# Optimization experiments

Measured on AMD Instinct MI355X. Metric: run time of the kernel, lower is better.

Reference implementation:

```python
import jax, jax.numpy as jnp
import numpy as np

N = 50000       # nodes per subgraph scale
E = 800000      # edges per subgraph scale
B = 4096        # number of subgraphs (graphs in the batch)
IN, HID, OUT = 64, 64, 32
NE = 8          # num_experts
EMB = 64        # emb_dim per expert
E2 = 131072     # graph-level edges for distortion loss


def setup_inputs() -> dict:
    key = jax.random.key(0)
    ks = jax.random.split(key, 16)
    inv = lambda d: 1.0 / np.sqrt(d)
    return {
        "subgraph_x0": jax.random.normal(ks[0], (N, IN), jnp.float32),
        "subgraph_x1": jax.random.normal(ks[1], (N, IN), jnp.float32),
        "W1": jax.random.normal(ks[2], (IN, HID), jnp.float32) * inv(IN),
        "b1": jnp.zeros((HID,), jnp.float32),
        "W2": jax.random.normal(ks[3], (HID, OUT), jnp.float32) * inv(HID),
        "b2": jnp.zeros((OUT,), jnp.float32),
        "Wc": jax.random.normal(ks[4], (OUT * 2, NE), jnp.float32) * inv(OUT * 2),
        "bc": jnp.zeros((NE,), jnp.float32),
        "embeddings": jax.random.normal(ks[5], (B, NE * EMB), jnp.float32),
        # precomputed shortest-path distances per graph edge (positive)
        "dis": jax.random.uniform(ks[6], (E2,), jnp.float32) * 1.5 + 0.5,
        "edge_index0": jax.random.randint(ks[7], (2, E), 0, N, jnp.int32),
        "edge_index1": jax.random.randint(ks[8], (2, E), 0, N, jnp.int32),
        "batch0": jnp.sort(jax.random.randint(ks[9], (N,), 0, B, jnp.int32)),
        "batch1": jnp.sort(jax.random.randint(ks[10], (N,), 0, B, jnp.int32)),
        "edge_index2": jax.random.randint(ks[11], (2, E2), 0, B, jnp.int32),
        "emb_dim": EMB,
    }


def _gcn_conv(x, W, b, src, dst, n):
    """PyG GCNConv: D^{-1/2}(A+I)D^{-1/2} X W + b, with self-loops."""
    xw = x @ W  # [n, out]
    ones = jnp.ones(src.shape, xw.dtype)
    deg = jax.ops.segment_sum(ones, dst, num_segments=n) + 1.0  # self-loop degree
    dinv = jax.lax.rsqrt(deg)  # [n]
    norm = dinv[src] * dinv[dst]  # [E]
    agg = jax.ops.segment_sum(xw[src] * norm[:, None], dst, num_segments=n)
    agg = agg + (dinv * dinv)[:, None] * xw  # self-loop messages
    return agg + b


def _mean_pool(x, batch, num_graphs):
    s = jax.ops.segment_sum(x, batch, num_segments=num_graphs)
    cnt = jax.ops.segment_sum(jnp.ones((x.shape[0],), x.dtype), batch,
                              num_segments=num_graphs)
    return s / jnp.maximum(cnt, 1.0)[:, None]


def _encode_scale(x, edge_index, batch, W1, b1, W2, b2, num_graphs):
    src, dst = edge_index[0], edge_index[1]
    n = x.shape[0]
    h = _gcn_conv(x, W1, b1, src, dst, n)
    h = _gcn_conv(h, W2, b2, src, dst, n)
    return _mean_pool(h, batch, num_graphs)


def reference(subgraph_x0, subgraph_x1, W1, b1, W2, b2, Wc, bc,
              embeddings, dis, edge_index0, edge_index1,
              batch0, batch1, edge_index2, emb_dim):
    num_graphs = embeddings.shape[0]
    x0 = _encode_scale(subgraph_x0, edge_index0, batch0, W1, b1, W2, b2, num_graphs)
    x1 = _encode_scale(subgraph_x1, edge_index1, batch1, W1, b1, W2, b2, num_graphs)
    x = jnp.concatenate([x0, x1], axis=-1)  # [B, 2*OUT]
    gate = jax.nn.softmax(x @ Wc + bc, axis=-1)  # temperature = 1.0

    # distortion loss over graph-level edges
    s, d = edge_index2[0], edge_index2[1]
    e = edge_index2.shape[1]
    diff = (embeddings[s] - embeddings[d]) ** 2  # [E2, NE*emb_dim]
    diff = diff.reshape(e, diff.shape[1] // emb_dim, emb_dim).sum(axis=2)  # [E2, NE]
    weights = jax.nn.softmax(gate[s] * gate[d], axis=1)  # [E2, NE]
    dsum = jnp.sum(diff * weights, axis=-1)  # [E2]
    loss_distortion = jnp.mean(jnp.abs(dsum / dis - 1.0))
    return gate, loss_distortion
```

## Files before the change

### kernel.cpp

```cpp
#include <hip/hip_runtime.h>
#include <math.h>

constexpr int IN_F  = 64;
constexpr int HID_F = 64;
constexpr int OUT_F = 32;
constexpr int NEXP  = 8;
constexpr int EMB   = 64;


__global__ void zero_f32_kernel(float* __restrict__ p, long long n) {
    long long i = (long long)blockIdx.x * blockDim.x + threadIdx.x;
    long long stride = (long long)gridDim.x * blockDim.x;
    for (; i < n; i += stride) p[i] = 0.0f;
}

__global__ void zero_i32_kernel(int* __restrict__ p, long long n) {
    long long i = (long long)blockIdx.x * blockDim.x + threadIdx.x;
    long long stride = (long long)gridDim.x * blockDim.x;
    for (; i < n; i += stride) p[i] = 0;
}

__global__ __launch_bounds__(1024)
void w12_kernel(const float* __restrict__ W1, const float* __restrict__ W2,
                const float* __restrict__ b1,
                float* __restrict__ W12, float* __restrict__ c1)
{
    __shared__ float sW2[HID_F * OUT_F];
    const int tid = threadIdx.x;
    for (int i = tid; i < HID_F * OUT_F; i += 1024) sW2[i] = W2[i];
    __syncthreads();
    for (int idx = tid; idx < IN_F * OUT_F; idx += 1024) {
        int i = idx >> 5, j = idx & 31;
        float acc = 0.0f;
#pragma unroll
        for (int k = 0; k < HID_F; ++k) acc += W1[i * HID_F + k] * sW2[k * OUT_F + j];
        W12[idx] = acc;
    }
    if (tid < OUT_F) {
        float acc = 0.0f;
#pragma unroll
        for (int k = 0; k < HID_F; ++k) acc += b1[k] * sW2[k * OUT_F + tid];
        c1[tid] = acc;
    }
}

__global__ void hist2_kernel(const int* __restrict__ ei0, const int* __restrict__ ei1,
                             int* __restrict__ counts, int E, int N)
{
    int e = blockIdx.x * blockDim.x + threadIdx.x;
    if (e >= 2 * E) return;
    int d = (e < E) ? ei0[E + e] : (ei1[E + (e - E)] + N);
    atomicAdd(&counts[d], 1);
}

__global__ __launch_bounds__(1024)
void scan1_kernel(const int* __restrict__ counts, int* __restrict__ lexcl,
                  int* __restrict__ partials, int N)
{
    __shared__ int wsum[16];
    const int tid  = threadIdx.x;
    const int lane = tid & 63;
    const int wv   = tid >> 6;
    const int i    = blockIdx.x * 1024 + tid;

    int v = (i < N) ? counts[i] : 0;
    int x = v;
#pragma unroll
    for (int off = 1; off < 64; off <<= 1) {
        int t = __shfl_up(x, off);
        if (lane >= off) x += t;
    }
    if (lane == 63) wsum[wv] = x;
    __syncthreads();
    int woff = 0;
    for (int w = 0; w < wv; ++w) woff += wsum[w];
    if (i < N) lexcl[i] = woff + x - v;
    if (tid == 1023) partials[blockIdx.x] = woff + x;
}

__global__ __launch_bounds__(1024)
void scan2_kernel(int* __restrict__ partials, int NB)
{
    __shared__ int wsum[16];
    const int tid  = threadIdx.x;
    const int lane = tid & 63;
    const int wv   = tid >> 6;
    int v = (tid < NB) ? partials[tid] : 0;
    int x = v;
#pragma unroll
    for (int off = 1; off < 64; off <<= 1) {
        int t = __shfl_up(x, off);
        if (lane >= off) x += t;
    }
    if (lane == 63) wsum[wv] = x;
    __syncthreads();
    int woff = 0;
    for (int w = 0; w < wv; ++w) woff += wsum[w];
    if (tid < NB) partials[tid] = woff + x - v;
}

__global__ void scan3_kernel(const int* __restrict__ lexcl, const int* __restrict__ partials,
                             const int* __restrict__ counts,
                             int* __restrict__ offsets, int* __restrict__ cursor,
                             float* __restrict__ dinv, int n2, int e2tot)
{
    int i = blockIdx.x * blockDim.x + threadIdx.x;
    if (i >= n2) return;
    int o = lexcl[i] + partials[i >> 10];
    offsets[i] = o;
    cursor[i]  = o;
    dinv[i] = rsqrtf((float)counts[i] + 1.0f);
    if (i == 0) offsets[n2] = e2tot;
}

__global__ __launch_bounds__(256)
void scatter2_shard_kernel(const int* __restrict__ ei0, const int* __restrict__ ei1,
                           int* __restrict__ cursor, int* __restrict__ csr_src,
                           int E, int N, int n2)
{
    const int shard   = blockIdx.x & 7;
    const int bid     = blockIdx.x >> 3;
    const int nblocks = gridDim.x >> 3;
    const int lo = (int)(((long long)n2 * shard) >> 3);
    const int hi = (int)(((long long)n2 * (shard + 1)) >> 3);

    long long start  = (long long)bid * blockDim.x + threadIdx.x;
    long long stride = (long long)nblocks * blockDim.x;
    const long long e2 = 2LL * E;
    for (long long e = start; e < e2; e += stride) {
        int s, d;
        if (e < E) { s = ei0[e];                 d = ei0[E + e]; }
        else       { s = ei1[e - E] + N;         d = ei1[E + (e - E)] + N; }
        if (d >= lo && d < hi) {
            int pos = atomicAdd(&cursor[d], 1);
            csr_src[pos] = s;
        }
    }
}

__global__ __launch_bounds__(256)
void gemm_ys2_kernel(const float* __restrict__ x0, const float* __restrict__ x1,
                     const float* __restrict__ W12, const float* __restrict__ dinv,
                     float* __restrict__ Ys, int N, int n2)
{
    __shared__ float Ws[IN_F * OUT_F];
    __shared__ float xs[8 * IN_F];
    const int tid = threadIdx.x;

    for (int i = tid; i < IN_F * OUT_F; i += 256) Ws[i] = W12[i];
    const int row0 = blockIdx.x * 8;
    for (int i = tid; i < 8 * IN_F; i += 256) {
        int r = i >> 6;
        int rr = row0 + r;
        float v = 0.0f;
        if (rr < n2) {
            v = (rr < N) ? x0[(size_t)rr * IN_F + (i & 63)]
                         : x1[(size_t)(rr - N) * IN_F + (i & 63)];
        }
        xs[i] = v;
    }
    __syncthreads();

    const int r = tid >> 5;
    const int c = tid & 31;
    const int row = row0 + r;
    if (row >= n2) return;

    float acc = 0.0f;
#pragma unroll
    for (int k = 0; k < IN_F; ++k) acc += xs[r * IN_F + k] * Ws[k * OUT_F + c];

    Ys[(size_t)row * OUT_F + c] = acc * dinv[row];
}

template<int MODE>
__global__ __launch_bounds__(256)
void csr_agg32_kernel(const int* __restrict__ csr_src, const int* __restrict__ offsets,
                      const float* __restrict__ in, const float* __restrict__ dinv,
                      float* __restrict__ sdsum, const float* __restrict__ c1,
                      const float* __restrict__ b2,
                      float* __restrict__ out, int n)
{
    constexpr int F = OUT_F;
    const int lane = threadIdx.x & 63;
    const int wid  = (blockIdx.x * (blockDim.x >> 6)) + (threadIdx.x >> 6);
    const int sub  = lane >> 5;
    const int f    = lane & 31;
    const int node = wid * 2 + sub;
    const int lbase = sub * F;

    const bool valid = (node < n);
    const int nc   = valid ? node : 0;
    const int off0 = offsets[nc];
    const int off1 = valid ? offsets[nc + 1] : off0;

    float acc0 = valid ? in[(size_t)nc * F + f] : 0.0f;
    float acc1 = 0.0f, acc2 = 0.0f, acc3 = 0.0f;
    float dsum = 0.0f;
    for (int k = off0; k < off1; k += F) {
        int nk = off1 - k; if (nk > F) nk = F;
        int sj = (f < nk) ? csr_src[k + f] : 0;
        if (MODE == 0) {
            float dv = dinv[sj];
            dsum += (f < nk) ? dv : 0.0f;
        }
        int t = 0;
        for (; t + 8 <= nk; t += 8) {
            int s0 = __shfl(sj, lbase + t);
            int s1 = __shfl(sj, lbase + t + 1);
            int s2 = __shfl(sj, lbase + t + 2);
            int s3 = __shfl(sj, lbase + t + 3);
            int s4 = __shfl(sj, lbase + t + 4);
            int s5 = __shfl(sj, lbase + t + 5);
            int s6 = __shfl(sj, lbase + t + 6);
            int s7 = __shfl(sj, lbase + t + 7);
            float v0 = in[(size_t)s0 * F + f];
            float v1 = in[(size_t)s1 * F + f];
            float v2 = in[(size_t)s2 * F + f];
            float v3 = in[(size_t)s3 * F + f];
            float v4 = in[(size_t)s4 * F + f];
            float v5 = in[(size_t)s5 * F + f];
            float v6 = in[(size_t)s6 * F + f];
            float v7 = in[(size_t)s7 * F + f];
            acc0 += v0 + v4;
            acc1 += v1 + v5;
            acc2 += v2 + v6;
            acc3 += v3 + v7;
        }
        for (; t < nk; ++t) {
            int s = __shfl(sj, lbase + t);
            acc0 += in[(size_t)s * F + f];
        }
    }
    if (MODE == 0) {
#pragma unroll
        for (int off = 1; off < 32; off <<= 1) dsum += __shfl_xor(dsum, off);
    }
    if (valid) {
        float di = dinv[node];
        float s = (acc0 + acc1) + (acc2 + acc3);
        if (MODE == 0) {
            out[(size_t)node * F + f] = di * di * s;
            if (f == 0) sdsum[node] = dsum;
        } else {
            float t = di * (di + sdsum[node]);
            out[(size_t)node * F + f] = di * s + t * c1[f] + b2[f];
        }
    }
}

__global__ void pool_sum2_kernel(const float* __restrict__ h,
                                 const int* __restrict__ bat0, const int* __restrict__ bat1,
                                 float* __restrict__ pooled, float* __restrict__ cnt,
                                 int N, int n2, int B)
{
    int t = blockIdx.x * blockDim.x + threadIdx.x;
    int i = t >> 5;
    int f = t & 31;
    if (i >= n2) return;
    int g = (i < N) ? bat0[i] : (bat1[i - N] + B);
    atomicAdd(&pooled[(size_t)g * OUT_F + f], h[(size_t)i * OUT_F + f]);
    if (f == 0) atomicAdd(&cnt[g], 1.0f);
}

__global__ void pool_div_kernel(float* __restrict__ pooled, const float* __restrict__ cnt, int B2)
{
    int t = blockIdx.x * blockDim.x + threadIdx.x;
    if (t >= B2 * OUT_F) return;
    int g = t >> 5;
    pooled[t] /= fmaxf(cnt[g], 1.0f);
}

__global__ void gate_kernel(const float* __restrict__ p0, const float* __restrict__ p1,
                            const float* __restrict__ Wc, const float* __restrict__ bc,
                            float* __restrict__ gate, int B)
{
    int g = blockIdx.x * blockDim.x + threadIdx.x;
    if (g >= B) return;
    float xv[2 * OUT_F];
#pragma unroll
    for (int k = 0; k < OUT_F; ++k) xv[k] = p0[(size_t)g * OUT_F + k];
#pragma unroll
    for (int k = 0; k < OUT_F; ++k) xv[OUT_F + k] = p1[(size_t)g * OUT_F + k];

    float lg[NEXP];
    float m = -1e30f;
#pragma unroll
    for (int e = 0; e < NEXP; ++e) {
        float acc = bc[e];
#pragma unroll
        for (int k = 0; k < 2 * OUT_F; ++k) acc += xv[k] * Wc[k * NEXP + e];
        lg[e] = acc;
        m = fmaxf(m, acc);
    }
    float se = 0.0f;
#pragma unroll
    for (int e = 0; e < NEXP; ++e) { lg[e] = expf(lg[e] - m); se += lg[e]; }
    float inv = 1.0f / se;
#pragma unroll
    for (int e = 0; e < NEXP; ++e) gate[(size_t)g * NEXP + e] = lg[e] * inv;
}

__global__ void zero_scalar_kernel(float* p) { *p = 0.0f; }

__global__ void histD_kernel(const int* __restrict__ s_idx, int* __restrict__ cntD, int E2) {
    int e = blockIdx.x * blockDim.x + threadIdx.x;
    if (e >= E2) return;
    atomicAdd(&cntD[s_idx[e]], 1);
}

__global__ void combineD_kernel(const int* __restrict__ lexclD, const int* __restrict__ partialsD,
                                int* __restrict__ offD, int* __restrict__ curD, int B, int E2)
{
    int i = blockIdx.x * blockDim.x + threadIdx.x;
    if (i >= B) return;
    int o = lexclD[i] + partialsD[i >> 10];
    offD[i] = o;
    curD[i] = o;
    if (i == 0) offD[B] = E2;
}

__global__ void scatterD_kernel(const int* __restrict__ s_idx, const int* __restrict__ d_idx,
                                const float* __restrict__ dis,
                                int* __restrict__ curD, int* __restrict__ dD,
                                float* __restrict__ disD, int E2)
{
    int e = blockIdx.x * blockDim.x + threadIdx.x;
    if (e >= E2) return;
    int s = s_idx[e];
    int pos = atomicAdd(&curD[s], 1);
    dD[pos] = d_idx[e];
    disD[pos] = dis[e];
}

__global__ __launch_bounds__(256)
void distortion3_kernel(const float* __restrict__ emb, const float* __restrict__ gate,
                        const int* __restrict__ offD, const int* __restrict__ dD,
                        const float* __restrict__ disD,
                        float* __restrict__ loss, int B, int E2)
{
    const int s    = (blockIdx.x * (blockDim.x >> 6)) + (threadIdx.x >> 6);
    const int lane = threadIdx.x & 63;
    const int half = lane >> 5;
    const int hl   = lane & 31;
    const int g    = hl >> 4;
    if (s >= B) return;

    const float4* emb4  = (const float4*)emb;
    const float4* gate4 = (const float4*)gate;

    const float4* es = emb4 + (size_t)s * 128;
    float4 a0 = es[hl];
    float4 a1 = es[hl + 32];
    float4 a2 = es[hl + 64];
    float4 a3 = es[hl + 96];
    float4 gs0 = gate4[(size_t)s * 2];
    float4 gs1 = gate4[(size_t)s * 2 + 1];

    float lsum = 0.0f;
    const int j0 = offD[s];
    const int j1 = offD[s + 1];
    for (int j = j0 + half; j < j1; j += 2) {
        int d = dD[j];
        float dv = disD[j];
        const float4* ed = emb4 + (size_t)d * 128;
        float4 b0 = ed[hl];
        float4 b1 = ed[hl + 32];
        float4 b2 = ed[hl + 64];
        float4 b3 = ed[hl + 96];
        float4 gd0 = gate4[(size_t)d * 2];
        float4 gd1 = gate4[(size_t)d * 2 + 1];

        float dx;
        float pa, pb, pc, pd;
        dx = a0.x - b0.x; pa  = dx * dx;
        dx = a0.y - b0.y; pa += dx * dx;
        dx = a0.z - b0.z; pa += dx * dx;
        dx = a0.w - b0.w; pa += dx * dx;
        dx = a1.x - b1.x; pb  = dx * dx;
        dx = a1.y - b1.y; pb += dx * dx;
        dx = a1.z - b1.z; pb += dx * dx;
        dx = a1.w - b1.w; pb += dx * dx;
        dx = a2.x - b2.x; pc  = dx * dx;
        dx = a2.y - b2.y; pc += dx * dx;
        dx = a2.z - b2.z; pc += dx * dx;
        dx = a2.w - b2.w; pc += dx * dx;
        dx = a3.x - b3.x; pd  = dx * dx;
        dx = a3.y - b3.y; pd += dx * dx;
        dx = a3.z - b3.z; pd += dx * dx;
        dx = a3.w - b3.w; pd += dx * dx;

#pragma unroll
        for (int off = 1; off < 16; off <<= 1) {
            pa += __shfl_xor(pa, off);
            pb += __shfl_xor(pb, off);
            pc += __shfl_xor(pc, off);
            pd += __shfl_xor(pd, off);
        }

        float gp[NEXP] = { gs0.x * gd0.x, gs0.y * gd0.y, gs0.z * gd0.z, gs0.w * gd0.w,
                           gs1.x * gd1.x, gs1.y * gd1.y, gs1.z * gd1.z, gs1.w * gd1.w };
        float m = gp[0];
#pragma unroll
        for (int j2 = 1; j2 < NEXP; ++j2) m = fmaxf(m, gp[j2]);
        float se = 0.0f;
#pragma unroll
        for (int j2 = 0; j2 < NEXP; ++j2) { gp[j2] = expf(gp[j2] - m); se += gp[j2]; }

        float v = pa * gp[g] + pb * gp[g + 2] + pc * gp[g + 4] + pd * gp[g + 6];
        v += __shfl_xor(v, 16);

        lsum += fabsf((v / se) / dv - 1.0f);
    }
    float other = __shfl_xor(lsum, 32);
    if (lane == 0) atomicAdd(loss, (lsum + other) / (float)E2);
}

extern "C" void kernel_launch(void* const* d_in, const int* in_sizes, int n_in,
                              void* d_out, int out_size, void* d_ws, size_t ws_size,
                              hipStream_t stream)
{
    const float* x0   = (const float*)d_in[0];
    const float* x1   = (const float*)d_in[1];
    const float* W1   = (const float*)d_in[2];
    const float* b1   = (const float*)d_in[3];
    const float* W2   = (const float*)d_in[4];
    const float* b2   = (const float*)d_in[5];
    const float* Wc   = (const float*)d_in[6];
    const float* bc   = (const float*)d_in[7];
    const float* emb  = (const float*)d_in[8];
    const float* dis  = (const float*)d_in[9];
    const int*   ei0  = (const int*)d_in[10];
    const int*   ei1  = (const int*)d_in[11];
    const int*   bat0 = (const int*)d_in[12];
    const int*   bat1 = (const int*)d_in[13];
    const int*   ei2  = (const int*)d_in[14];

    const int N  = in_sizes[0] / IN_F;
    const int E  = in_sizes[10] / 2;
    const int B  = in_sizes[8] / (NEXP * EMB);
    const int E2 = in_sizes[14] / 2;
    const int n2 = 2 * N;

    float* gate_out = (float*)d_out;
    float* loss_out = gate_out + (size_t)B * NEXP;

    float* ws      = (float*)d_ws;
    float* dinv    = ws;
    float* Ys      = dinv + n2;
    float* Zs      = Ys + (size_t)n2 * OUT_F;
    float* sdsum   = Zs + (size_t)n2 * OUT_F;
    float* pooled  = sdsum + n2;
    float* cnt     = pooled + (size_t)2 * B * OUT_F;
    float* W12     = cnt + 2 * B;
    float* c1      = W12 + IN_F * OUT_F;
    float* disD    = c1 + OUT_F;
    int*   iws     = (int*)(disD + E2);
    int*   counts  = iws;
    int*   offsets = counts + n2;
    int*   cursor  = offsets + n2 + 1;
    int*   csr_src = cursor + n2;
    int*   lexcl   = csr_src + 2 * E;
    int*   partials= lexcl + n2;
    int*   cntD    = partials + 1024;
    int*   lexclD  = cntD + B;
    int*   partialsD = lexclD + B;
    int*   offD    = partialsD + 16;
    int*   curD    = offD + B + 1;
    int*   dD      = curD + B;

    const int TB = 256;
    const int zgrid = 512;
    const int NB2 = (n2 + 1023) / 1024;
    const int NBD = (B + 1023) / 1024;

    w12_kernel<<<1, 1024, 0, stream>>>(W1, W2, b1, W12, c1);

    zero_i32_kernel<<<zgrid, TB, 0, stream>>>(counts, n2);
    hist2_kernel<<<(2 * E + TB - 1) / TB, TB, 0, stream>>>(ei0, ei1, counts, E, N);
    scan1_kernel<<<NB2, 1024, 0, stream>>>(counts, lexcl, partials, n2);
    scan2_kernel<<<1, 1024, 0, stream>>>(partials, NB2);
    scan3_kernel<<<(n2 + TB - 1) / TB, TB, 0, stream>>>(lexcl, partials, counts,
                                                        offsets, cursor, dinv, n2, 2 * E);
    scatter2_shard_kernel<<<1024, TB, 0, stream>>>(ei0, ei1, cursor, csr_src, E, N, n2);

    zero_i32_kernel<<<zgrid, TB, 0, stream>>>(cntD, B);
    histD_kernel<<<(E2 + TB - 1) / TB, TB, 0, stream>>>(ei2, cntD, E2);
    scan1_kernel<<<NBD, 1024, 0, stream>>>(cntD, lexclD, partialsD, B);
    scan2_kernel<<<1, 1024, 0, stream>>>(partialsD, NBD);
    combineD_kernel<<<(B + TB - 1) / TB, TB, 0, stream>>>(lexclD, partialsD, offD, curD, B, E2);
    scatterD_kernel<<<(E2 + TB - 1) / TB, TB, 0, stream>>>(ei2, ei2 + E2, dis,
                                                           curD, dD, disD, E2);

    gemm_ys2_kernel<<<(n2 + 7) / 8, 256, 0, stream>>>(x0, x1, W12, dinv, Ys, N, n2);
    csr_agg32_kernel<0><<<(n2 + 7) / 8, TB, 0, stream>>>(csr_src, offsets, Ys, dinv,
                                                         sdsum, nullptr, nullptr, Zs, n2);
    csr_agg32_kernel<1><<<(n2 + 7) / 8, TB, 0, stream>>>(csr_src, offsets, Zs, dinv,
                                                         sdsum, c1, b2, Ys, n2);

    zero_f32_kernel<<<zgrid, TB, 0, stream>>>(pooled, (long long)2 * B * OUT_F);
    zero_f32_kernel<<<zgrid, TB, 0, stream>>>(cnt, 2 * B);
    pool_sum2_kernel<<<((n2 * 32) + TB - 1) / TB, TB, 0, stream>>>(Ys, bat0, bat1,
                                                                   pooled, cnt, N, n2, B);
    pool_div_kernel<<<((2 * B * OUT_F) + TB - 1) / TB, TB, 0, stream>>>(pooled, cnt, 2 * B);

    gate_kernel<<<(B + TB - 1) / TB, TB, 0, stream>>>(pooled, pooled + (size_t)B * OUT_F,
                                                      Wc, bc, gate_out, B);

    zero_scalar_kernel<<<1, 1, 0, stream>>>(loss_out);
    distortion3_kernel<<<(B + 3) / 4, TB, 0, stream>>>(emb, gate_out, offD, dD, disD,
                                                       loss_out, B, E2);
}
```

Measured before the change: 419.8 us.

## Bucket distortion edges by destination quarter and pin quarters to XCDs

Graph-level edges are now bucketed by (destination quarter, source) instead of source alone, using a 4*B-entry histogram, scan and scatter. The distortion kernel launches a fixed 1024 blocks and derives a quarter and half-range from blockIdx&7. Blocks on the same XCD (assuming round-robin block placement) then gather destination embeddings from one quarter of the table, which should improve per-XCD L2 hit rates. In exchange, each source's embedding row and gate are reloaded up to four times, and the bucketing scan is four times larger.

```diff
diff --git a/kernel.cpp b/kernel.cpp
--- a/kernel.cpp
+++ b/kernel.cpp
@@ -303,114 +303,131 @@
 
 __global__ void zero_scalar_kernel(float* p) { *p = 0.0f; }
 
-__global__ void histD_kernel(const int* __restrict__ s_idx, int* __restrict__ cntD, int E2) {
+__global__ void histK_kernel(const int* __restrict__ s_idx, const int* __restrict__ d_idx,
+                             int* __restrict__ histK, int E2, int B, int quarter)
+{
     int e = blockIdx.x * blockDim.x + threadIdx.x;
     if (e >= E2) return;
-    atomicAdd(&cntD[s_idx[e]], 1);
-}
-
-__global__ void combineD_kernel(const int* __restrict__ lexclD, const int* __restrict__ partialsD,
-                                int* __restrict__ offD, int* __restrict__ curD, int B, int E2)
+    int qd = d_idx[e] / quarter; if (qd > 3) qd = 3;
+    atomicAdd(&histK[qd * B + s_idx[e]], 1);
+}
+
+__global__ void combineK_kernel(const int* __restrict__ lexclK, const int* __restrict__ partialsK,
+                                int* __restrict__ offK, int* __restrict__ curK, int nk, int E2)
 {
     int i = blockIdx.x * blockDim.x + threadIdx.x;
-    if (i >= B) return;
-    int o = lexclD[i] + partialsD[i >> 10];
-    offD[i] = o;
-    curD[i] = o;
-    if (i == 0) offD[B] = E2;
-}
-
-__global__ void scatterD_kernel(const int* __restrict__ s_idx, const int* __restrict__ d_idx,
+    if (i >= nk) return;
+    int o = lexclK[i] + partialsK[i >> 10];
+    offK[i] = o;
+    curK[i] = o;
+    if (i == 0) offK[nk] = E2;
+}
+
+__global__ void scatterK_kernel(const int* __restrict__ s_idx, const int* __restrict__ d_idx,
                                 const float* __restrict__ dis,
-                                int* __restrict__ curD, int* __restrict__ dD,
-                                float* __restrict__ disD, int E2)
+                                int* __restrict__ curK, int* __restrict__ dD,
+                                float* __restrict__ disD, int E2, int B, int quarter)
 {
     int e = blockIdx.x * blockDim.x + threadIdx.x;
     if (e >= E2) return;
-    int s = s_idx[e];
-    int pos = atomicAdd(&curD[s], 1);
-    dD[pos] = d_idx[e];
+    int d = d_idx[e];
+    int qd = d / quarter; if (qd > 3) qd = 3;
+    int pos = atomicAdd(&curK[qd * B + s_idx[e]], 1);
+    dD[pos] = d;
     disD[pos] = dis[e];
 }
 
 __global__ __launch_bounds__(256)
-void distortion3_kernel(const float* __restrict__ emb, const float* __restrict__ gate,
-                        const int* __restrict__ offD, const int* __restrict__ dD,
+void distortion5_kernel(const float* __restrict__ emb, const float* __restrict__ gate,
+                        const int* __restrict__ offK, const int* __restrict__ dD,
                         const float* __restrict__ disD,
                         float* __restrict__ loss, int B, int E2)
 {
-    const int s    = (blockIdx.x * (blockDim.x >> 6)) + (threadIdx.x >> 6);
     const int lane = threadIdx.x & 63;
     const int half = lane >> 5;
     const int hl   = lane & 31;
     const int g    = hl >> 4;
-    if (s >= B) return;
+    const int xcd  = blockIdx.x & 7;
+    const int bid  = blockIdx.x >> 3;
+    const int wv   = threadIdx.x >> 6;
+    const int wIdx = bid * 4 + wv;
+
+    const int qd   = xcd >> 1;
+    const int sh   = xcd & 1;
+    const int halfB = B >> 1;
+    const int k0 = qd * B + sh * halfB;
+    const int k1 = qd * B + (sh ? B : halfB);
 
     const float4* emb4  = (const float4*)emb;
     const float4* gate4 = (const float4*)gate;
 
-    const float4* es = emb4 + (size_t)s * 128;
-    float4 a0 = es[hl];
-    float4 a1 = es[hl + 32];
-    float4 a2 = es[hl + 64];
-    float4 a3 = es[hl + 96];
-    float4 gs0 = gate4[(size_t)s * 2];
-    float4 gs1 = gate4[(size_t)s * 2 + 1];
-
     float lsum = 0.0f;
-    const int j0 = offD[s];
-    const int j1 = offD[s + 1];
-    for (int j = j0 + half; j < j1; j += 2) {
-        int d = dD[j];
-        float dv = disD[j];
-        const float4* ed = emb4 + (size_t)d * 128;
-        float4 b0 = ed[hl];
-        float4 b1 = ed[hl + 32];
-        float4 b2 = ed[hl + 64];
-        float4 b3 = ed[hl + 96];
-        float4 gd0 = gate4[(size_t)d * 2];
-        float4 gd1 = gate4[(size_t)d * 2 + 1];
-
-        float dx;
-        float pa, pb, pc, pd;
-        dx = a0.x - b0.x; pa  = dx * dx;
-        dx = a0.y - b0.y; pa += dx * dx;
-        dx = a0.z - b0.z; pa += dx * dx;
-        dx = a0.w - b0.w; pa += dx * dx;
-        dx = a1.x - b1.x; pb  = dx * dx;
-        dx = a1.y - b1.y; pb += dx * dx;
-        dx = a1.z - b1.z; pb += dx * dx;
-        dx = a1.w - b1.w; pb += dx * dx;
-        dx = a2.x - b2.x; pc  = dx * dx;
-        dx = a2.y - b2.y; pc += dx * dx;
-        dx = a2.z - b2.z; pc += dx * dx;
-        dx = a2.w - b2.w; pc += dx * dx;
-        dx = a3.x - b3.x; pd  = dx * dx;
-        dx = a3.y - b3.y; pd += dx * dx;
-        dx = a3.z - b3.z; pd += dx * dx;
-        dx = a3.w - b3.w; pd += dx * dx;
-
-#pragma unroll
-        for (int off = 1; off < 16; off <<= 1) {
-            pa += __shfl_xor(pa, off);
-            pb += __shfl_xor(pb, off);
-            pc += __shfl_xor(pc, off);
-            pd += __shfl_xor(pd, off);
-        }
-
-        float gp[NEXP] = { gs0.x * gd0.x, gs0.y * gd0.y, gs0.z * gd0.z, gs0.w * gd0.w,
-                           gs1.x * gd1.x, gs1.y * gd1.y, gs1.z * gd1.z, gs1.w * gd1.w };
-        float m = gp[0];
-#pragma unroll
-        for (int j2 = 1; j2 < NEXP; ++j2) m = fmaxf(m, gp[j2]);
-        float se = 0.0f;
-#pragma unroll
-        for (int j2 = 0; j2 < NEXP; ++j2) { gp[j2] = expf(gp[j2] - m); se += gp[j2]; }
-
-        float v = pa * gp[g] + pb * gp[g + 2] + pc * gp[g + 4] + pd * gp[g + 6];
-        v += __shfl_xor(v, 16);
-
-        lsum += fabsf((v / se) / dv - 1.0f);
+    for (int k = k0 + wIdx; k < k1; k += 512) {
+        const int j0 = offK[k];
+        const int j1 = offK[k + 1];
+        if (j0 == j1) continue;
+        const int s = k - qd * B;
+
+        const float4* es = emb4 + (size_t)s * 128;
+        float4 a0 = es[hl];
+        float4 a1 = es[hl + 32];
+        float4 a2 = es[hl + 64];
+        float4 a3 = es[hl + 96];
+        float4 gs0 = gate4[(size_t)s * 2];
+        float4 gs1 = gate4[(size_t)s * 2 + 1];
+
+        for (int j = j0 + half; j < j1; j += 2) {
+            int d = dD[j];
+            float dv = disD[j];
+            const float4* ed = emb4 + (size_t)d * 128;
+            float4 b0 = ed[hl];
+            float4 b1 = ed[hl + 32];
+            float4 b2 = ed[hl + 64];
+            float4 b3 = ed[hl + 96];
+            float4 gd0 = gate4[(size_t)d * 2];
+            float4 gd1 = gate4[(size_t)d * 2 + 1];
+
+            float dx;
+            float pa, pb, pc, pd;
+            dx = a0.x - b0.x; pa  = dx * dx;
+            dx = a0.y - b0.y; pa += dx * dx;
+            dx = a0.z - b0.z; pa += dx * dx;
+            dx = a0.w - b0.w; pa += dx * dx;
+            dx = a1.x - b1.x; pb  = dx * dx;
+            dx = a1.y - b1.y; pb += dx * dx;
+            dx = a1.z - b1.z; pb += dx * dx;
+            dx = a1.w - b1.w; pb += dx * dx;
+            dx = a2.x - b2.x; pc  = dx * dx;
+            dx = a2.y - b2.y; pc += dx * dx;
+            dx = a2.z - b2.z; pc += dx * dx;
+            dx = a2.w - b2.w; pc += dx * dx;
+            dx = a3.x - b3.x; pd  = dx * dx;
+            dx = a3.y - b3.y; pd += dx * dx;
+            dx = a3.z - b3.z; pd += dx * dx;
+            dx = a3.w - b3.w; pd += dx * dx;
+
+#pragma unroll
+            for (int off = 1; off < 16; off <<= 1) {
+                pa += __shfl_xor(pa, off);
+                pb += __shfl_xor(pb, off);
+                pc += __shfl_xor(pc, off);
+                pd += __shfl_xor(pd, off);
+            }
+
+            float gp[NEXP] = { gs0.x * gd0.x, gs0.y * gd0.y, gs0.z * gd0.z, gs0.w * gd0.w,
+                               gs1.x * gd1.x, gs1.y * gd1.y, gs1.z * gd1.z, gs1.w * gd1.w };
+            float m = gp[0];
+#pragma unroll
+            for (int j2 = 1; j2 < NEXP; ++j2) m = fmaxf(m, gp[j2]);
+            float se = 0.0f;
+#pragma unroll
+            for (int j2 = 0; j2 < NEXP; ++j2) { gp[j2] = expf(gp[j2] - m); se += gp[j2]; }
+
+            float v = pa * gp[g] + pb * gp[g + 2] + pc * gp[g + 4] + pd * gp[g + 6];
+            v += __shfl_xor(v, 16);
+
+            lsum += fabsf((v / se) / dv - 1.0f);
+        }
     }
     float other = __shfl_xor(lsum, 32);
     if (lane == 0) atomicAdd(loss, (lsum + other) / (float)E2);
@@ -441,6 +458,8 @@
     const int B  = in_sizes[8] / (NEXP * EMB);
     const int E2 = in_sizes[14] / 2;
     const int n2 = 2 * N;
+    const int nk = 4 * B;
+    const int quarter = (B + 3) / 4;
 
     float* gate_out = (float*)d_out;
     float* loss_out = gate_out + (size_t)B * NEXP;
@@ -462,17 +481,17 @@
     int*   csr_src = cursor + n2;
     int*   lexcl   = csr_src + 2 * E;
     int*   partials= lexcl + n2;
-    int*   cntD    = partials + 1024;
-    int*   lexclD  = cntD + B;
-    int*   partialsD = lexclD + B;
-    int*   offD    = partialsD + 16;
-    int*   curD    = offD + B + 1;
-    int*   dD      = curD + B;
+    int*   histK   = partials + 1024;
+    int*   lexclK  = histK + nk;
+    int*   partialsK = lexclK + nk;
+    int*   offK    = partialsK + 1024;
+    int*   curK    = offK + nk + 1;
+    int*   dD      = curK + nk;
 
     const int TB = 256;
     const int zgrid = 512;
     const int NB2 = (n2 + 1023) / 1024;
-    const int NBD = (B + 1023) / 1024;
+    const int NBK = (nk + 1023) / 1024;
 
     w12_kernel<<<1, 1024, 0, stream>>>(W1, W2, b1, W12, c1);
 
@@ -484,13 +503,13 @@
                                                         offsets, cursor, dinv, n2, 2 * E);
     scatter2_shard_kernel<<<1024, TB, 0, stream>>>(ei0, ei1, cursor, csr_src, E, N, n2);
 
-    zero_i32_kernel<<<zgrid, TB, 0, stream>>>(cntD, B);
-    histD_kernel<<<(E2 + TB - 1) / TB, TB, 0, stream>>>(ei2, cntD, E2);
-    scan1_kernel<<<NBD, 1024, 0, stream>>>(cntD, lexclD, partialsD, B);
-    scan2_kernel<<<1, 1024, 0, stream>>>(partialsD, NBD);
-    combineD_kernel<<<(B + TB - 1) / TB, TB, 0, stream>>>(lexclD, partialsD, offD, curD, B, E2);
-    scatterD_kernel<<<(E2 + TB - 1) / TB, TB, 0, stream>>>(ei2, ei2 + E2, dis,
-                                                           curD, dD, disD, E2);
+    zero_i32_kernel<<<zgrid, TB, 0, stream>>>(histK, nk);
+    histK_kernel<<<(E2 + TB - 1) / TB, TB, 0, stream>>>(ei2, ei2 + E2, histK, E2, B, quarter);
+    scan1_kernel<<<NBK, 1024, 0, stream>>>(histK, lexclK, partialsK, nk);
+    scan2_kernel<<<1, 1024, 0, stream>>>(partialsK, NBK);
+    combineK_kernel<<<(nk + TB - 1) / TB, TB, 0, stream>>>(lexclK, partialsK, offK, curK, nk, E2);
+    scatterK_kernel<<<(E2 + TB - 1) / TB, TB, 0, stream>>>(ei2, ei2 + E2, dis,
+                                                           curK, dD, disD, E2, B, quarter);
 
     gemm_ys2_kernel<<<(n2 + 7) / 8, 256, 0, stream>>>(x0, x1, W12, dinv, Ys, N, n2);
     csr_agg32_kernel<0><<<(n2 + 7) / 8, TB, 0, stream>>>(csr_src, offsets, Ys, dinv,
@@ -508,6 +527,6 @@
                                                       Wc, bc, gate_out, B);
 
     zero_scalar_kernel<<<1, 1, 0, stream>>>(loss_out);
-    distortion3_kernel<<<(B + 3) / 4, TB, 0, stream>>>(emb, gate_out, offD, dD, disD,
-                                                       loss_out, B, E2);
-}
+    distortion5_kernel<<<1024, TB, 0, stream>>>(emb, gate_out, offK, dD, disD,
+                                                loss_out, B, E2);
+}
```

Result: no change. 413.8 us (-1.4%).
